# Kernel optimization log

Measured on AMD Instinct MI355X. Metric: run time of the kernel, lower is better.

The kernel has to match this reference:

```python
import jax, jax.numpy as jnp
from jax import lax
import numpy as np

B, T, H, P = 256, 2048, 256, 24

def setup_inputs() -> dict:
    key = jax.random.key(0)
    ks = jax.random.split(key, 7)
    s_ih = 1.0 / np.sqrt(H)
    return {
        "x": jax.random.normal(ks[0], (B, T, 1), dtype=jnp.float32),
        "W_ih": jax.random.normal(ks[1], (H, 1), dtype=jnp.float32) * s_ih,
        "W_hh": jax.random.normal(ks[2], (H, H), dtype=jnp.float32) * s_ih,
        "b_ih": jax.random.normal(ks[3], (H,), dtype=jnp.float32) * s_ih,
        "b_hh": jax.random.normal(ks[4], (H,), dtype=jnp.float32) * s_ih,
        "W_out": jax.random.normal(ks[5], (P, H), dtype=jnp.float32) * s_ih,
        "b_out": jax.random.normal(ks[6], (P,), dtype=jnp.float32) * s_ih,
    }

def reference(x, W_ih, W_hh, b_ih, b_hh, W_out, b_out):
    # Precompute input projection for all timesteps: [B,T,H]
    xp = jnp.einsum('bti,hi->bth', x, W_ih) + b_ih + b_hh
    h0 = jnp.zeros((x.shape[0], W_hh.shape[0]), dtype=x.dtype)

    def step(h, xt):  # xt: [B,H]
        h_new = jnp.tanh(xt + h @ W_hh.T)
        return h_new, None

    hT, _ = lax.scan(step, h0, xp.transpose(1, 0, 2))  # scan over T
    # Linear head on last hidden state: [B,P]
    return hT @ W_out.T + b_out
```

## Files before the change

### kernel.cpp

```cpp
#include <hip/hip_runtime.h>


#define BB 256
#define TT 2048
#define HH 256
#define PP 24
#define HSTR 20

typedef float v2f __attribute__((ext_vector_type(2)));

struct alignas(16) hquad { v2f lo, hi; };

__device__ __forceinline__ int hidx(int k) { return (k >> 4) * HSTR + (k & 15); }

template<int CTRL>
__device__ __forceinline__ float dppadd(float dst, float src) {
    return dst + __int_as_float(__builtin_amdgcn_update_dpp(
        0, __float_as_int(src), CTRL, 0xf, 0xf, true));
}

__global__ __launch_bounds__(512, 1)
void rnn_persist(const float* __restrict__ x,
                 const float* __restrict__ W_ih,
                 const float* __restrict__ W_hh,
                 const float* __restrict__ b_ih,
                 const float* __restrict__ b_hh,
                 const float* __restrict__ W_out,
                 const float* __restrict__ b_out,
                 float* __restrict__ out)
{
    __shared__ __align__(16) float hbuf[2][16 * HSTR];

    const int tid = threadIdx.x;
    const int b   = blockIdx.x;
    const int c   = tid & 15;
    const int g   = tid >> 4;

    hbuf[0][hidx(tid & 255)] = 0.0f;

    const int m[8] = {0, 2, 7, 5, 8, 10, 15, 13};

    v2f w2[8][8];
    #pragma unroll
    for (int s = 0; s < 8; ++s) {
        const int row_idx = 8 * g + ((c ^ m[s]) >> 1);
        const float* row = W_hh + row_idx * HH + 16 * c;
        #pragma unroll
        for (int j = 0; j < 4; ++j) {
            const float4 q = *(const float4*)(row + 4 * j);
            w2[s][2 * j + 0] = (v2f){q.x, q.y};
            w2[s][2 * j + 1] = (v2f){q.z, q.w};
        }
    }

    const int   o_fin = 8 * g + (c >> 1);
    const float wih   = W_ih[o_fin];
    const float cb    = b_ih[o_fin] + b_hh[o_fin];
    const int   widx  = hidx(o_fin);

    __syncthreads();

    const float* hc0 = hbuf[0] + c * HSTR;
    const float* hc1 = hbuf[1] + c * HSTR;
    const float* xb  = x + b * TT;

    auto step = [&](const float* __restrict__ cur, float* __restrict__ nxt,
                    float xt) __attribute__((always_inline)) {
        const hquad* hq = (const hquad*)cur;
        const hquad q0 = hq[0], q1 = hq[1], q2 = hq[2], q3 = hq[3];

        v2f acc[8];
        #pragma unroll
        for (int s = 0; s < 8; ++s) acc[s] = w2[s][0] * q0.lo;
        #pragma unroll
        for (int s = 0; s < 8; ++s)
            acc[s] = __builtin_elementwise_fma(w2[s][1], q0.hi, acc[s]);
        #pragma unroll
        for (int s = 0; s < 8; ++s)
            acc[s] = __builtin_elementwise_fma(w2[s][2], q1.lo, acc[s]);
        #pragma unroll
        for (int s = 0; s < 8; ++s)
            acc[s] = __builtin_elementwise_fma(w2[s][3], q1.hi, acc[s]);
        #pragma unroll
        for (int s = 0; s < 8; ++s)
            acc[s] = __builtin_elementwise_fma(w2[s][4], q2.lo, acc[s]);
        #pragma unroll
        for (int s = 0; s < 8; ++s)
            acc[s] = __builtin_elementwise_fma(w2[s][5], q2.hi, acc[s]);
        #pragma unroll
        for (int s = 0; s < 8; ++s)
            acc[s] = __builtin_elementwise_fma(w2[s][6], q3.lo, acc[s]);
        #pragma unroll
        for (int s = 0; s < 8; ++s)
            acc[s] = __builtin_elementwise_fma(w2[s][7], q3.hi, acc[s]);

        float aa[8];
        #pragma unroll
        for (int s = 0; s < 8; ++s) aa[s] = acc[s].x + acc[s].y;

        float b0 = dppadd<0x128>(aa[0], aa[4]);
        float b1 = dppadd<0x128>(aa[1], aa[5]);
        float b2 = dppadd<0x128>(aa[2], aa[6]);
        float b3 = dppadd<0x128>(aa[3], aa[7]);
        float c0 = dppadd<0x141>(b0, b2);
        float c1 = dppadd<0x141>(b1, b3);
        float d  = dppadd<0x4E>(c0, c1);
        float e  = dppadd<0xB1>(d, d);

        const float u  = fmaf(xt, wih, cb) + e;
        const float p  = __builtin_amdgcn_exp2f(u * 2.8853900817779268f);
        const float th = fmaf(-2.f, __builtin_amdgcn_rcpf(p + 1.f), 1.f);
        nxt[widx] = th;
        __syncthreads();
    };

    float4 xa = *(const float4*)(xb + 0);
    float4 xc = *(const float4*)(xb + 4);
    for (int t = 0; t < TT; t += 8) {
        const int tn = (t + 8 < TT) ? (t + 8) : t;
        const float4 xa_n = *(const float4*)(xb + tn);
        const float4 xc_n = *(const float4*)(xb + tn + 4);
        step(hc0, hbuf[1], xa.x);
        step(hc1, hbuf[0], xa.y);
        step(hc0, hbuf[1], xa.z);
        step(hc1, hbuf[0], xa.w);
        step(hc0, hbuf[1], xc.x);
        step(hc1, hbuf[0], xc.y);
        step(hc0, hbuf[1], xc.z);
        step(hc1, hbuf[0], xc.w);
        xa = xa_n;
        xc = xc_n;
    }

    if (tid < PP) {
        const float* wo = W_out + tid * HH;
        float s0 = 0.f, s1 = 0.f, s2 = 0.f, s3 = 0.f;
        #pragma unroll
        for (int h = 0; h < HH; h += 4) {
            s0 = fmaf(wo[h + 0], hbuf[0][hidx(h + 0)], s0);
            s1 = fmaf(wo[h + 1], hbuf[0][hidx(h + 1)], s1);
            s2 = fmaf(wo[h + 2], hbuf[0][hidx(h + 2)], s2);
            s3 = fmaf(wo[h + 3], hbuf[0][hidx(h + 3)], s3);
        }
        out[b * PP + tid] = b_out[tid] + (s0 + s1) + (s2 + s3);
    }
}

extern "C" void kernel_launch(void* const* d_in, const int* in_sizes, int n_in,
                              void* d_out, int out_size, void* d_ws, size_t ws_size,
                              hipStream_t stream) {
    const float* x     = (const float*)d_in[0];
    const float* W_ih  = (const float*)d_in[1];
    const float* W_hh  = (const float*)d_in[2];
    const float* b_ih  = (const float*)d_in[3];
    const float* b_hh  = (const float*)d_in[4];
    const float* W_out = (const float*)d_in[5];
    const float* b_out = (const float*)d_in[6];
    float* out = (float*)d_out;

    rnn_persist<<<BB, 512, 0, stream>>>(x, W_ih, W_hh, b_ih, b_hh, W_out, b_out, out);
}
```

Before: 967.2 us.

## Split each hidden-state dot product across wave halves with permlane32 cross-half reduction

Re-partitions the recurrent matvec so each lane covers 8 columns of hidden state for two output-row blocks, instead of 16 columns for one block. Each step then reads half as much hidden state from LDS per lane. The split sums are combined across the two 32-lane halves of a wave with permlane32_swap, falling back to a shuffle when that builtin is unavailable. In exchange, each lane runs two DPP reduction trees and a cross-half exchange per step, which lengthens the serial dependency chain on each timestep.

```diff
diff --git a/kernel.cpp b/kernel.cpp
--- a/kernel.cpp
+++ b/kernel.cpp
@@ -8,6 +8,7 @@
 #define HSTR 20
 
 typedef float v2f __attribute__((ext_vector_type(2)));
+typedef int   v2i __attribute__((ext_vector_type(2)));
 
 struct alignas(16) hquad { v2f lo, hi; };
 
@@ -17,6 +18,16 @@
 __device__ __forceinline__ float dppadd(float dst, float src) {
     return dst + __int_as_float(__builtin_amdgcn_update_dpp(
         0, __float_as_int(src), CTRL, 0xf, 0xf, true));
+}
+
+__device__ __forceinline__ float xhalf_sum(float e) {
+#if __has_builtin(__builtin_amdgcn_permlane32_swap)
+    const int ei = __float_as_int(e);
+    v2i pr = __builtin_amdgcn_permlane32_swap(ei, ei, false, false);
+    return __int_as_float(pr.x) + __int_as_float(pr.y);
+#else
+    return e + __shfl_xor(e, 32, 64);
+#endif
 }
 
 __global__ __launch_bounds__(512, 1)
@@ -33,79 +44,99 @@
 
     const int tid = threadIdx.x;
     const int b   = blockIdx.x;
-    const int c   = tid & 15;
-    const int g   = tid >> 4;
+    const int L   = tid & 63;
+    const int c4  = L & 15;
+    const int r0  = (L >> 4) & 1;
+    const int d4  = L >> 5;
+    const int r   = (tid >> 6) * 2 + r0;
+    const int d   = d4 * 16 + c4;
 
     hbuf[0][hidx(tid & 255)] = 0.0f;
 
     const int m[8] = {0, 2, 7, 5, 8, 10, 15, 13};
 
-    v2f w2[8][8];
+    v2f w2[2][8][4];
     #pragma unroll
-    for (int s = 0; s < 8; ++s) {
-        const int row_idx = 8 * g + ((c ^ m[s]) >> 1);
-        const float* row = W_hh + row_idx * HH + 16 * c;
+    for (int bk = 0; bk < 2; ++bk) {
         #pragma unroll
-        for (int j = 0; j < 4; ++j) {
-            const float4 q = *(const float4*)(row + 4 * j);
-            w2[s][2 * j + 0] = (v2f){q.x, q.y};
-            w2[s][2 * j + 1] = (v2f){q.z, q.w};
+        for (int s = 0; s < 8; ++s) {
+            const int row_idx = 16 * r + 8 * bk + ((c4 ^ m[s]) >> 1);
+            const float* row = W_hh + row_idx * HH + 8 * d;
+            const float4 qA = *(const float4*)(row);
+            const float4 qB = *(const float4*)(row + 4);
+            w2[bk][s][0] = (v2f){qA.x, qA.y};
+            w2[bk][s][1] = (v2f){qA.z, qA.w};
+            w2[bk][s][2] = (v2f){qB.x, qB.y};
+            w2[bk][s][3] = (v2f){qB.z, qB.w};
         }
     }
 
-    const int   o_fin = 8 * g + (c >> 1);
+    const int   o_fin = 16 * r + 8 * d4 + (c4 >> 1);
     const float wih   = W_ih[o_fin];
     const float cb    = b_ih[o_fin] + b_hh[o_fin];
     const int   widx  = hidx(o_fin);
 
     __syncthreads();
 
-    const float* hc0 = hbuf[0] + c * HSTR;
-    const float* hc1 = hbuf[1] + c * HSTR;
+    const float* hc0 = hbuf[0] + (d >> 1) * HSTR + (d & 1) * 8;
+    const float* hc1 = hbuf[1] + (d >> 1) * HSTR + (d & 1) * 8;
     const float* xb  = x + b * TT;
 
     auto step = [&](const float* __restrict__ cur, float* __restrict__ nxt,
                     float xt) __attribute__((always_inline)) {
         const hquad* hq = (const hquad*)cur;
-        const hquad q0 = hq[0], q1 = hq[1], q2 = hq[2], q3 = hq[3];
+        const hquad qa = hq[0], qb = hq[1];
 
-        v2f acc[8];
+        v2f acc0[8], acc1[8];
         #pragma unroll
-        for (int s = 0; s < 8; ++s) acc[s] = w2[s][0] * q0.lo;
+        for (int s = 0; s < 8; ++s) acc0[s] = w2[0][s][0] * qa.lo;
+        #pragma unroll
+        for (int s = 0; s < 8; ++s) acc1[s] = w2[1][s][0] * qa.lo;
         #pragma unroll
         for (int s = 0; s < 8; ++s)
-            acc[s] = __builtin_elementwise_fma(w2[s][1], q0.hi, acc[s]);
+            acc0[s] = __builtin_elementwise_fma(w2[0][s][1], qa.hi, acc0[s]);
         #pragma unroll
         for (int s = 0; s < 8; ++s)
-            acc[s] = __builtin_elementwise_fma(w2[s][2], q1.lo, acc[s]);
+            acc1[s] = __builtin_elementwise_fma(w2[1][s][1], qa.hi, acc1[s]);
         #pragma unroll
         for (int s = 0; s < 8; ++s)
-            acc[s] = __builtin_elementwise_fma(w2[s][3], q1.hi, acc[s]);
+            acc0[s] = __builtin_elementwise_fma(w2[0][s][2], qb.lo, acc0[s]);
         #pragma unroll
         for (int s = 0; s < 8; ++s)
-            acc[s] = __builtin_elementwise_fma(w2[s][4], q2.lo, acc[s]);
+            acc1[s] = __builtin_elementwise_fma(w2[1][s][2], qb.lo, acc1[s]);
         #pragma unroll
         for (int s = 0; s < 8; ++s)
-            acc[s] = __builtin_elementwise_fma(w2[s][5], q2.hi, acc[s]);
+            acc0[s] = __builtin_elementwise_fma(w2[0][s][3], qb.hi, acc0[s]);
         #pragma unroll
         for (int s = 0; s < 8; ++s)
-            acc[s] = __builtin_elementwise_fma(w2[s][6], q3.lo, acc[s]);
+            acc1[s] = __builtin_elementwise_fma(w2[1][s][3], qb.hi, acc1[s]);
+
+        float aa0[8], aa1[8];
         #pragma unroll
-        for (int s = 0; s < 8; ++s)
-            acc[s] = __builtin_elementwise_fma(w2[s][7], q3.hi, acc[s]);
+        for (int s = 0; s < 8; ++s) aa0[s] = acc0[s].x + acc0[s].y;
+        #pragma unroll
+        for (int s = 0; s < 8; ++s) aa1[s] = acc1[s].x + acc1[s].y;
 
-        float aa[8];
-        #pragma unroll
-        for (int s = 0; s < 8; ++s) aa[s] = acc[s].x + acc[s].y;
+        float b00 = dppadd<0x128>(aa0[0], aa0[4]);
+        float b01 = dppadd<0x128>(aa0[1], aa0[5]);
+        float b02 = dppadd<0x128>(aa0[2], aa0[6]);
+        float b03 = dppadd<0x128>(aa0[3], aa0[7]);
+        float c00 = dppadd<0x141>(b00, b02);
+        float c01 = dppadd<0x141>(b01, b03);
+        float d0  = dppadd<0x4E>(c00, c01);
+        float e0  = dppadd<0xB1>(d0, d0);
+        float b10 = dppadd<0x128>(aa1[0], aa1[4]);
+        float b11 = dppadd<0x128>(aa1[1], aa1[5]);
+        float b12 = dppadd<0x128>(aa1[2], aa1[6]);
+        float b13 = dppadd<0x128>(aa1[3], aa1[7]);
+        float c10 = dppadd<0x141>(b10, b12);
+        float c11 = dppadd<0x141>(b11, b13);
+        float d1  = dppadd<0x4E>(c10, c11);
+        float e1  = dppadd<0xB1>(d1, d1);
 
-        float b0 = dppadd<0x128>(aa[0], aa[4]);
-        float b1 = dppadd<0x128>(aa[1], aa[5]);
-        float b2 = dppadd<0x128>(aa[2], aa[6]);
-        float b3 = dppadd<0x128>(aa[3], aa[7]);
-        float c0 = dppadd<0x141>(b0, b2);
-        float c1 = dppadd<0x141>(b1, b3);
-        float d  = dppadd<0x4E>(c0, c1);
-        float e  = dppadd<0xB1>(d, d);
+        const float full0 = xhalf_sum(e0);
+        const float full1 = xhalf_sum(e1);
+        const float e     = d4 ? full1 : full0;
 
         const float u  = fmaf(xt, wih, cb) + e;
         const float p  = __builtin_amdgcn_exp2f(u * 2.8853900817779268f);
```

Result: slower. 1.134 ms (+17.2%).
